# Optimization experiments

Hardware: AMD Instinct MI355X
Metric: run time of the kernel (lower is better)

Reference implementation:

```python
import jax, jax.numpy as jnp
import numpy as np

IN = 128          # in_channels
STEPS = 3         # processing_steps


def setup_inputs() -> dict:
    key = jax.random.key(0)
    ks = jax.random.split(key, 6)
    N, B = 500000, 1024
    x = jax.random.normal(ks[0], (N, IN), dtype=jnp.float32)
    batch = jnp.sort(jax.random.randint(ks[1], (N,), 0, B)).astype(jnp.int64)
    s = 1.0 / np.sqrt(IN)  # PyTorch LSTM init range
    w_ih = jax.random.uniform(ks[2], (4 * IN, 2 * IN), jnp.float32, -s, s)
    w_hh = jax.random.uniform(ks[3], (4 * IN, IN), jnp.float32, -s, s)
    b_ih = jax.random.uniform(ks[4], (4 * IN,), jnp.float32, -s, s)
    b_hh = jax.random.uniform(ks[5], (4 * IN,), jnp.float32, -s, s)
    return {"x": x, "w_ih": w_ih, "w_hh": w_hh, "b_ih": b_ih, "b_hh": b_hh,
            "batch": batch, "batch_size": B}


def reference(x, w_ih, w_hh, b_ih, b_hh, batch, batch_size):
    h = jnp.zeros((batch_size, IN), x.dtype)
    c = jnp.zeros((batch_size, IN), x.dtype)
    q_star = jnp.zeros((batch_size, 2 * IN), x.dtype)
    for _ in range(STEPS):
        # single-layer LSTM step (PyTorch gate order: i, f, g, o)
        gates = q_star @ w_ih.T + b_ih + h @ w_hh.T + b_hh
        i, f, g, o = jnp.split(gates, 4, axis=-1)
        c = jax.nn.sigmoid(f) * c + jax.nn.sigmoid(i) * jnp.tanh(g)
        h = jax.nn.sigmoid(o) * jnp.tanh(c)
        q = h  # [B, IN]
        # per-graph segment softmax over attention scores
        e = jnp.sum(x * q[batch], axis=-1)                       # [N]
        m = jax.ops.segment_max(e, batch, num_segments=batch_size)
        ex = jnp.exp(e - m[batch])
        denom = jax.ops.segment_sum(ex, batch, num_segments=batch_size)
        a = ex / denom[batch]                                    # [N]
        # weighted segment-sum readout
        r = jax.ops.segment_sum(x * a[:, None], batch, num_segments=batch_size)
        q_star = jnp.concatenate([q, r], axis=-1)                # [B, 2*IN]
    return q_star
```

## Files before the change

### kernel.cpp

```cpp
#include <hip/hip_runtime.h>
#include <math.h>

#define IN_CH 128
#define G4    512
#define K1    256

__device__ __forceinline__ float sigmoidf_(float v){ return 1.f/(1.f + expf(-v)); }

__device__ __forceinline__ float dot4_(float4 a, float4 b){
  return a.x*b.x + a.y*b.y + a.z*b.z + a.w*b.w;
}

__device__ __forceinline__ float reduce32_(float v){
  int t;
  t = __builtin_amdgcn_update_dpp(0, __float_as_int(v), 0xB1, 0xF, 0xF, true);
  v += __int_as_float(t);
  t = __builtin_amdgcn_update_dpp(0, __float_as_int(v), 0x4E, 0xF, 0xF, true);
  v += __int_as_float(t);
  t = __builtin_amdgcn_update_dpp(0, __float_as_int(v), 0x141, 0xF, 0xF, true);
  v += __int_as_float(t);
  t = __builtin_amdgcn_update_dpp(0, __float_as_int(v), 0x140, 0xF, 0xF, true);
  v += __int_as_float(t);
  t = __builtin_amdgcn_ds_swizzle(__float_as_int(v), 0x401F);
  return v + __int_as_float(t);
}

__global__ void prologue_kernel(const float* __restrict__ w_ih, const float* __restrict__ w_hh,
                                float* __restrict__ wTih, float* __restrict__ wThh,
                                const int* __restrict__ batch, int N, int B, int* __restrict__ segs,
                                const float* __restrict__ b_ih, const float* __restrict__ b_hh,
                                float* __restrict__ h, float* __restrict__ c, float* __restrict__ qstar){
  int blk = blockIdx.x;
  if (blk < 512){
    int idx = blk*256 + threadIdx.x;
    { int g = idx / K1; int k = idx - g*K1; wTih[k*G4 + g] = w_ih[idx]; }
    if (idx < G4*IN_CH){ int g = idx / IN_CH; int k = idx - g*IN_CH; wThh[k*G4 + g] = w_hh[idx]; }
  } else if (blk < 517){
    int b = (blk - 512)*256 + threadIdx.x;
    if (b > B) return;
    if (b == B){ segs[B] = N; return; }
    int lo = 0, hi = N;
    while (lo < hi){ int mid = (lo + hi) >> 1; if (batch[mid] < b) lo = mid + 1; else hi = mid; }
    segs[b] = lo;
  } else {
    int idx = (blk - 517)*256 + threadIdx.x;
    if (idx >= B*IN_CH) return;
    int b = idx >> 7, ch = idx & 127;
    float iv = sigmoidf_(b_ih[ch]           + b_hh[ch]);
    float gv = tanhf    (b_ih[2*IN_CH + ch] + b_hh[2*IN_CH + ch]);
    float ov = sigmoidf_(b_ih[3*IN_CH + ch] + b_hh[3*IN_CH + ch]);
    float cv = iv*gv;
    float hv = ov*tanhf(cv);
    c[idx] = cv; h[idx] = hv;
    qstar[b*K1 + ch] = hv;
  }
}

__global__ __launch_bounds__(512) void lstm_fused_kernel(
    const float* __restrict__ qstar_in, float* __restrict__ h, float* __restrict__ c,
    const float* __restrict__ wTih, const float* __restrict__ wThh,
    const float* __restrict__ b_ih, const float* __restrict__ b_hh,
    float* __restrict__ qstar_out){
  int g    = threadIdx.x;
  int row0 = blockIdx.x*8;
  __shared__ float qs[8][K1];
  __shared__ float hs[8][IN_CH];
  __shared__ float gs[8][G4];
  for (int t = g; t < 8*K1; t += 512){ int r = t >> 8; int k = t & 255; qs[r][k] = qstar_in[(row0+r)*K1 + k]; }
  for (int t = g; t < 8*IN_CH; t += 512){ int r = t >> 7; int k = t & 127; hs[r][k] = h[(row0+r)*IN_CH + k]; }
  __syncthreads();
  float bias = b_ih[g] + b_hh[g];
  float acc[8];
#pragma unroll
  for (int r = 0; r < 8; ++r) acc[r] = bias;
  for (int k4 = 0; k4 < K1/4; ++k4){
    float w0 = wTih[(4*k4+0)*G4 + g];
    float w1 = wTih[(4*k4+1)*G4 + g];
    float w2 = wTih[(4*k4+2)*G4 + g];
    float w3 = wTih[(4*k4+3)*G4 + g];
#pragma unroll
    for (int r = 0; r < 8; ++r){
      float4 q = *reinterpret_cast<const float4*>(&qs[r][4*k4]);
      acc[r] += q.x*w0 + q.y*w1 + q.z*w2 + q.w*w3;
    }
  }
  for (int k4 = 0; k4 < IN_CH/4; ++k4){
    float w0 = wThh[(4*k4+0)*G4 + g];
    float w1 = wThh[(4*k4+1)*G4 + g];
    float w2 = wThh[(4*k4+2)*G4 + g];
    float w3 = wThh[(4*k4+3)*G4 + g];
#pragma unroll
    for (int r = 0; r < 8; ++r){
      float4 hv = *reinterpret_cast<const float4*>(&hs[r][4*k4]);
      acc[r] += hv.x*w0 + hv.y*w1 + hv.z*w2 + hv.w*w3;
    }
  }
#pragma unroll
  for (int r = 0; r < 8; ++r) gs[r][g] = acc[r];
  __syncthreads();
  for (int t = g; t < 8*IN_CH; t += 512){
    int r = t >> 7, ch = t & 127;
    int idx = (row0+r)*IN_CH + ch;
    float iv = sigmoidf_(gs[r][ch]);
    float fv = sigmoidf_(gs[r][IN_CH + ch]);
    float gv = tanhf(gs[r][2*IN_CH + ch]);
    float ov = sigmoidf_(gs[r][3*IN_CH + ch]);
    float cv = fv*c[idx] + iv*gv;
    float hv = ov*tanhf(cv);
    c[idx] = cv; h[idx] = hv;
    qstar_out[(row0+r)*K1 + ch] = hv;
  }
}

__global__ __launch_bounds__(256) void attn_kernel(const float* __restrict__ x,
    float* __restrict__ qstar, const int* __restrict__ segs){
  int b = blockIdx.x;
  int s = segs[b], ce = segs[b+1];
  int jmax = (ce > 0) ? (ce - 1) : 0;
  int tid = threadIdx.x;
  int wave = tid >> 6, lane = tid & 63;
  int hh = lane >> 5, l32 = lane & 31;
  const float4* x4 = reinterpret_cast<const float4*>(x);
  const float4* q4 = reinterpret_cast<const float4*>(&qstar[(size_t)b*K1]);
  float4 qv = q4[l32];

  float m = -INFINITY, d = 0.f;
  float4 acc = make_float4(0.f,0.f,0.f,0.f);

  const int WSTR = 32;
  int jw = s + wave*8;

  float4 A0,A1,A2,A3, B0,B1,B2,B3, C0,C1,C2,C3;

#define LOADW(R0,R1,R2,R3,WB_)                                   \
  {                                                              \
    int r0 = min((WB_) + 0 + hh, jmax);                          \
    int r1 = min((WB_) + 2 + hh, jmax);                          \
    int r2 = min((WB_) + 4 + hh, jmax);                          \
    int r3 = min((WB_) + 6 + hh, jmax);                          \
    R0 = x4[(size_t)r0*(IN_CH/4) + l32];                         \
    R1 = x4[(size_t)r1*(IN_CH/4) + l32];                         \
    R2 = x4[(size_t)r2*(IN_CH/4) + l32];                         \
    R3 = x4[(size_t)r3*(IN_CH/4) + l32];                         \
  }

#define COMP(R0,R1,R2,R3,WB_)                                    \
  {                                                              \
    float e0 = dot4_(R0, qv);                                    \
    float e1 = dot4_(R1, qv);                                    \
    float e2 = dot4_(R2, qv);                                    \
    float e3 = dot4_(R3, qv);                                    \
    e0 = reduce32_(e0); e1 = reduce32_(e1);                      \
    e2 = reduce32_(e2); e3 = reduce32_(e3);                      \
    e0 = ((WB_) + 0 + hh < ce) ? e0 : -INFINITY;                 \
    e1 = ((WB_) + 2 + hh < ce) ? e1 : -INFINITY;                 \
    e2 = ((WB_) + 4 + hh < ce) ? e2 : -INFINITY;                 \
    e3 = ((WB_) + 6 + hh < ce) ? e3 : -INFINITY;                 \
    float em = fmaxf(fmaxf(e0,e1), fmaxf(e2,e3));                \
    if (em > m){                                                 \
      float corr = __expf(m - em);                               \
      d *= corr;                                                 \
      acc.x *= corr; acc.y *= corr; acc.z *= corr; acc.w *= corr;\
      m = em;                                                    \
    }                                                            \
    float p0 = (e0 == -INFINITY) ? 0.f : __expf(e0 - m);         \
    float p1 = (e1 == -INFINITY) ? 0.f : __expf(e1 - m);         \
    float p2 = (e2 == -INFINITY) ? 0.f : __expf(e2 - m);         \
    float p3 = (e3 == -INFINITY) ? 0.f : __expf(e3 - m);         \
    d += (p0 + p1) + (p2 + p3);                                  \
    acc.x += p0*R0.x + p1*R1.x + p2*R2.x + p3*R3.x;              \
    acc.y += p0*R0.y + p1*R1.y + p2*R2.y + p3*R3.y;              \
    acc.z += p0*R0.z + p1*R1.z + p2*R2.z + p3*R3.z;              \
    acc.w += p0*R0.w + p1*R1.w + p2*R2.w + p3*R3.w;              \
  }

  LOADW(A0,A1,A2,A3, jw)
  LOADW(B0,B1,B2,B3, jw + WSTR)
  for (;;){
    if (jw >= ce) break;
    LOADW(C0,C1,C2,C3, jw + 2*WSTR)
    COMP (A0,A1,A2,A3, jw)
    jw += WSTR;
    if (jw >= ce) break;
    LOADW(A0,A1,A2,A3, jw + 2*WSTR)
    COMP (B0,B1,B2,B3, jw)
    jw += WSTR;
    if (jw >= ce) break;
    LOADW(B0,B1,B2,B3, jw + 2*WSTR)
    COMP (C0,C1,C2,C3, jw)
    jw += WSTR;
  }
#undef LOADW
#undef COMP

  {
    float mo = __shfl_xor(m, 32), dd = __shfl_xor(d, 32);
    float ox = __shfl_xor(acc.x, 32), oy = __shfl_xor(acc.y, 32);
    float oz = __shfl_xor(acc.z, 32), ow = __shfl_xor(acc.w, 32);
    float mn = fmaxf(m, mo);
    float c1 = (mn == -INFINITY) ? 0.f : __expf(m - mn);
    float c2 = (mn == -INFINITY) ? 0.f : __expf(mo - mn);
    d = d*c1 + dd*c2;
    acc.x = acc.x*c1 + ox*c2; acc.y = acc.y*c1 + oy*c2;
    acc.z = acc.z*c1 + oz*c2; acc.w = acc.w*c1 + ow*c2;
    m = mn;
  }
  __shared__ float mbuf[4], dbuf[4];
  __shared__ float rbuf[4][IN_CH];
  if (lane < 32){
    *reinterpret_cast<float4*>(&rbuf[wave][l32*4]) = acc;
    if (l32 == 0){ mbuf[wave] = m; dbuf[wave] = d; }
  }
  __syncthreads();
  if (tid < IN_CH){
    float M = fmaxf(fmaxf(mbuf[0], mbuf[1]), fmaxf(mbuf[2], mbuf[3]));
    float f0 = (M == -INFINITY) ? 0.f : __expf(mbuf[0] - M);
    float f1 = (M == -INFINITY) ? 0.f : __expf(mbuf[1] - M);
    float f2 = (M == -INFINITY) ? 0.f : __expf(mbuf[2] - M);
    float f3 = (M == -INFINITY) ? 0.f : __expf(mbuf[3] - M);
    float R = rbuf[0][tid]*f0 + rbuf[1][tid]*f1 + rbuf[2][tid]*f2 + rbuf[3][tid]*f3;
    float D = dbuf[0]*f0 + dbuf[1]*f1 + dbuf[2]*f2 + dbuf[3]*f3;
    qstar[(size_t)b*K1 + IN_CH + tid] = (D > 0.f) ? R/D : 0.f;
  }
}

extern "C" void kernel_launch(void* const* d_in, const int* in_sizes, int n_in,
                              void* d_out, int out_size, void* d_ws, size_t ws_size,
                              hipStream_t stream){
  const float* x     = (const float*)d_in[0];
  const float* w_ih  = (const float*)d_in[1];
  const float* w_hh  = (const float*)d_in[2];
  const float* b_ih  = (const float*)d_in[3];
  const float* b_hh  = (const float*)d_in[4];
  const int*   batch = (const int*)d_in[5];
  int N = in_sizes[0] / IN_CH;
  int B = out_size / K1;
  float* out = (float*)d_out;

  float* ws    = (float*)d_ws;
  float* h     = ws;
  float* c     = h + (size_t)B*IN_CH;
  float* wTih  = c + (size_t)B*IN_CH;
  float* wThh  = wTih + K1*G4;
  int*   segs  = (int*)(wThh + IN_CH*G4);

  prologue_kernel<<<517 + (B*IN_CH + 255)/256, 256, 0, stream>>>(
      w_ih, w_hh, wTih, wThh, batch, N, B, segs, b_ih, b_hh, h, c, out);

  attn_kernel<<<B, 256, 0, stream>>>(x, out, segs);
  for (int step = 1; step < 3; ++step){
    lstm_fused_kernel<<<B/8, 512, 0, stream>>>(out, h, c, wTih, wThh, b_ih, b_hh, out);
    attn_kernel<<<B, 256, 0, stream>>>(x, out, segs);
  }
}
```

Baseline: 200.1 us.

## Fold prologue into attention kernel, compute segment bounds in-kernel, use nontemporal x loads

Removes the separate prologue launch. Weight transposition and the initial LSTM-state computation move into the first attention launch, and each block finds its own segment bounds with a wave-wide 64-ary ballot search over the sorted batch array. The separate h buffer is dropped because h is read directly from the q_star output. Loads of x become nontemporal to reduce cache pollution. The cost is a redundant bound search in every attention launch and extra per-block bias-activation work on the first step.

```diff
diff --git a/kernel.cpp b/kernel.cpp
--- a/kernel.cpp
+++ b/kernel.cpp
@@ -11,6 +11,16 @@
   return a.x*b.x + a.y*b.y + a.z*b.z + a.w*b.w;
 }
 
+typedef float vf4_ __attribute__((ext_vector_type(4)));
+__device__ __forceinline__ float4 ntload4_(const float4* p){
+#if __has_builtin(__builtin_nontemporal_load)
+  vf4_ v = __builtin_nontemporal_load(reinterpret_cast<const vf4_*>(p));
+  return make_float4(v.x, v.y, v.z, v.w);
+#else
+  return *p;
+#endif
+}
+
 __device__ __forceinline__ float reduce32_(float v){
   int t;
   t = __builtin_amdgcn_update_dpp(0, __float_as_int(v), 0xB1, 0xF, 0xF, true);
@@ -25,49 +35,34 @@
   return v + __int_as_float(t);
 }
 
-__global__ void prologue_kernel(const float* __restrict__ w_ih, const float* __restrict__ w_hh,
-                                float* __restrict__ wTih, float* __restrict__ wThh,
-                                const int* __restrict__ batch, int N, int B, int* __restrict__ segs,
-                                const float* __restrict__ b_ih, const float* __restrict__ b_hh,
-                                float* __restrict__ h, float* __restrict__ c, float* __restrict__ qstar){
-  int blk = blockIdx.x;
-  if (blk < 512){
-    int idx = blk*256 + threadIdx.x;
-    { int g = idx / K1; int k = idx - g*K1; wTih[k*G4 + g] = w_ih[idx]; }
-    if (idx < G4*IN_CH){ int g = idx / IN_CH; int k = idx - g*IN_CH; wThh[k*G4 + g] = w_hh[idx]; }
-  } else if (blk < 517){
-    int b = (blk - 512)*256 + threadIdx.x;
-    if (b > B) return;
-    if (b == B){ segs[B] = N; return; }
-    int lo = 0, hi = N;
-    while (lo < hi){ int mid = (lo + hi) >> 1; if (batch[mid] < b) lo = mid + 1; else hi = mid; }
-    segs[b] = lo;
-  } else {
-    int idx = (blk - 517)*256 + threadIdx.x;
-    if (idx >= B*IN_CH) return;
-    int b = idx >> 7, ch = idx & 127;
-    float iv = sigmoidf_(b_ih[ch]           + b_hh[ch]);
-    float gv = tanhf    (b_ih[2*IN_CH + ch] + b_hh[2*IN_CH + ch]);
-    float ov = sigmoidf_(b_ih[3*IN_CH + ch] + b_hh[3*IN_CH + ch]);
-    float cv = iv*gv;
-    float hv = ov*tanhf(cv);
-    c[idx] = cv; h[idx] = hv;
-    qstar[b*K1 + ch] = hv;
-  }
+__device__ __forceinline__ int lbound64_(const int* __restrict__ batch,
+                                         int lo, int hi, int v, int lane){
+  while (hi - lo > 64){
+    int span = hi - lo;
+    int idx = lo + (int)(((long long)span * lane) >> 6);
+    int val = batch[idx];
+    unsigned long long mask = __ballot(val < v);
+    int k = (int)__popcll(mask);
+    int nlo = (k == 0)  ? lo : (lo + (int)(((long long)span * (k-1)) >> 6) + 1);
+    int nhi = (k == 64) ? hi : (lo + (int)(((long long)span * k) >> 6));
+    lo = nlo; hi = nhi;
+  }
+  int idx = lo + lane;
+  int val = (idx < hi) ? batch[idx] : 0x7fffffff;
+  unsigned long long mask = __ballot(val < v);
+  return lo + (int)__popcll(mask);
 }
 
 __global__ __launch_bounds__(512) void lstm_fused_kernel(
-    const float* __restrict__ qstar_in, float* __restrict__ h, float* __restrict__ c,
+    const float* __restrict__ qstar_in, float* __restrict__ c,
     const float* __restrict__ wTih, const float* __restrict__ wThh,
     const float* __restrict__ b_ih, const float* __restrict__ b_hh,
-    float* __restrict__ qstar_out){
+    float* __restrict__ qstar_out, int first){
   int g    = threadIdx.x;
   int row0 = blockIdx.x*8;
   __shared__ float qs[8][K1];
-  __shared__ float hs[8][IN_CH];
   __shared__ float gs[8][G4];
   for (int t = g; t < 8*K1; t += 512){ int r = t >> 8; int k = t & 255; qs[r][k] = qstar_in[(row0+r)*K1 + k]; }
-  for (int t = g; t < 8*IN_CH; t += 512){ int r = t >> 7; int k = t & 127; hs[r][k] = h[(row0+r)*IN_CH + k]; }
   __syncthreads();
   float bias = b_ih[g] + b_hh[g];
   float acc[8];
@@ -91,7 +86,7 @@
     float w3 = wThh[(4*k4+3)*G4 + g];
 #pragma unroll
     for (int r = 0; r < 8; ++r){
-      float4 hv = *reinterpret_cast<const float4*>(&hs[r][4*k4]);
+      float4 hv = *reinterpret_cast<const float4*>(&qs[r][4*k4]);
       acc[r] += hv.x*w0 + hv.y*w1 + hv.z*w2 + hv.w*w3;
     }
   }
@@ -101,28 +96,73 @@
   for (int t = g; t < 8*IN_CH; t += 512){
     int r = t >> 7, ch = t & 127;
     int idx = (row0+r)*IN_CH + ch;
+    float cprev;
+    if (first){
+      float iv0 = sigmoidf_(b_ih[ch] + b_hh[ch]);
+      float gv0 = tanhf(b_ih[2*IN_CH + ch] + b_hh[2*IN_CH + ch]);
+      cprev = iv0*gv0;
+    } else {
+      cprev = c[idx];
+    }
     float iv = sigmoidf_(gs[r][ch]);
     float fv = sigmoidf_(gs[r][IN_CH + ch]);
     float gv = tanhf(gs[r][2*IN_CH + ch]);
     float ov = sigmoidf_(gs[r][3*IN_CH + ch]);
-    float cv = fv*c[idx] + iv*gv;
+    float cv = fv*cprev + iv*gv;
     float hv = ov*tanhf(cv);
-    c[idx] = cv; h[idx] = hv;
+    c[idx] = cv;
     qstar_out[(row0+r)*K1 + ch] = hv;
   }
 }
 
-__global__ __launch_bounds__(256) void attn_kernel(const float* __restrict__ x,
-    float* __restrict__ qstar, const int* __restrict__ segs){
+__global__ __launch_bounds__(256) void attn_kernel(
+    const float* __restrict__ x, const int* __restrict__ batch, int N,
+    float* __restrict__ qstar,
+    const float* __restrict__ b_ih, const float* __restrict__ b_hh,
+    const float* __restrict__ w_ih, const float* __restrict__ w_hh,
+    float* __restrict__ wTih, float* __restrict__ wThh, int first){
   int b = blockIdx.x;
-  int s = segs[b], ce = segs[b+1];
+  int tid = threadIdx.x;
+  int lane = tid & 63, wave = tid >> 6;
+  int hh = lane >> 5, l32 = lane & 31;
+
+  if (first){
+    int gid = b*256 + tid;
+    if (gid < G4*K1){
+      int g = gid / K1, k = gid - g*K1; wTih[k*G4 + g] = w_ih[gid];
+    } else {
+      int gid2 = gid - G4*K1;
+      if (gid2 < G4*IN_CH){ int g = gid2 / IN_CH, k = gid2 - g*IN_CH; wThh[k*G4 + g] = w_hh[gid2]; }
+    }
+  }
+
+  int s  = lbound64_(batch, 0, N, b,   lane);
+  int ce = lbound64_(batch, s, N, b+1, lane);
   int jmax = (ce > 0) ? (ce - 1) : 0;
-  int tid = threadIdx.x;
-  int wave = tid >> 6, lane = tid & 63;
-  int hh = lane >> 5, l32 = lane & 31;
+
   const float4* x4 = reinterpret_cast<const float4*>(x);
-  const float4* q4 = reinterpret_cast<const float4*>(&qstar[(size_t)b*K1]);
-  float4 qv = q4[l32];
+  float4 qv;
+  if (first){
+    float hv4[4];
+#pragma unroll
+    for (int u = 0; u < 4; ++u){
+      int ch = l32*4 + u;
+      float iv = sigmoidf_(b_ih[ch]           + b_hh[ch]);
+      float gv = tanhf    (b_ih[2*IN_CH + ch] + b_hh[2*IN_CH + ch]);
+      float ov = sigmoidf_(b_ih[3*IN_CH + ch] + b_hh[3*IN_CH + ch]);
+      hv4[u] = ov*tanhf(iv*gv);
+    }
+    qv = make_float4(hv4[0], hv4[1], hv4[2], hv4[3]);
+    if (tid < IN_CH){
+      int ch = tid;
+      float iv = sigmoidf_(b_ih[ch]           + b_hh[ch]);
+      float gv = tanhf    (b_ih[2*IN_CH + ch] + b_hh[2*IN_CH + ch]);
+      float ov = sigmoidf_(b_ih[3*IN_CH + ch] + b_hh[3*IN_CH + ch]);
+      qstar[(size_t)b*K1 + ch] = ov*tanhf(iv*gv);
+    }
+  } else {
+    qv = reinterpret_cast<const float4*>(&qstar[(size_t)b*K1])[l32];
+  }
 
   float m = -INFINITY, d = 0.f;
   float4 acc = make_float4(0.f,0.f,0.f,0.f);
@@ -138,10 +178,10 @@
     int r1 = min((WB_) + 2 + hh, jmax);                          \
     int r2 = min((WB_) + 4 + hh, jmax);                          \
     int r3 = min((WB_) + 6 + hh, jmax);                          \
-    R0 = x4[(size_t)r0*(IN_CH/4) + l32];                         \
-    R1 = x4[(size_t)r1*(IN_CH/4) + l32];                         \
-    R2 = x4[(size_t)r2*(IN_CH/4) + l32];                         \
-    R3 = x4[(size_t)r3*(IN_CH/4) + l32];                         \
+    R0 = ntload4_(&x4[(size_t)r0*(IN_CH/4) + l32]);              \
+    R1 = ntload4_(&x4[(size_t)r1*(IN_CH/4) + l32]);              \
+    R2 = ntload4_(&x4[(size_t)r2*(IN_CH/4) + l32]);              \
+    R3 = ntload4_(&x4[(size_t)r3*(IN_CH/4) + l32]);              \
   }
 
 #define COMP(R0,R1,R2,R3,WB_)                                    \
@@ -237,19 +277,13 @@
   int B = out_size / K1;
   float* out = (float*)d_out;
 
-  float* ws    = (float*)d_ws;
-  float* h     = ws;
-  float* c     = h + (size_t)B*IN_CH;
-  float* wTih  = c + (size_t)B*IN_CH;
-  float* wThh  = wTih + K1*G4;
-  int*   segs  = (int*)(wThh + IN_CH*G4);
-
-  prologue_kernel<<<517 + (B*IN_CH + 255)/256, 256, 0, stream>>>(
-      w_ih, w_hh, wTih, wThh, batch, N, B, segs, b_ih, b_hh, h, c, out);
-
-  attn_kernel<<<B, 256, 0, stream>>>(x, out, segs);
-  for (int step = 1; step < 3; ++step){
-    lstm_fused_kernel<<<B/8, 512, 0, stream>>>(out, h, c, wTih, wThh, b_ih, b_hh, out);
-    attn_kernel<<<B, 256, 0, stream>>>(x, out, segs);
-  }
-}
+  float* wTih = (float*)d_ws;
+  float* wThh = wTih + K1*G4;
+  float* c    = wThh + IN_CH*G4;
+
+  attn_kernel<<<B, 256, 0, stream>>>(x, batch, N, out, b_ih, b_hh, w_ih, w_hh, wTih, wThh, 1);
+  lstm_fused_kernel<<<B/8, 512, 0, stream>>>(out, c, wTih, wThh, b_ih, b_hh, out, 1);
+  attn_kernel<<<B, 256, 0, stream>>>(x, batch, N, out, b_ih, b_hh, w_ih, w_hh, wTih, wThh, 0);
+  lstm_fused_kernel<<<B/8, 512, 0, stream>>>(out, c, wTih, wThh, b_ih, b_hh, out, 0);
+  attn_kernel<<<B, 256, 0, stream>>>(x, batch, N, out, b_ih, b_hh, w_ih, w_hh, wTih, wThh, 0);
+}
```

Result: slower. 233.7 us (+16.8%).
